# Kernel tuning notes

Hardware: AMD Instinct MI355X
Metric: run time of the kernel (lower is better)

## Reference

```python
import jax, jax.numpy as jnp
import numpy as np

NUM_EXPERTS = 64
INPUT_SIZE = 2048
NUM_TOKENS = 16384
TOPK = 8
INIT_STD = 0.02


def setup_inputs() -> dict:
    key = jax.random.key(0)
    k1, k2 = jax.random.split(key)
    input = jax.random.normal(k1, (NUM_TOKENS, INPUT_SIZE), dtype=jnp.float32)
    weight = INIT_STD * jax.random.normal(k2, (NUM_EXPERTS, INPUT_SIZE), dtype=jnp.float32)
    return {"input": input, "weight": weight}


def reference(input, weight):
    # gating GEMM: [N, D] x [E, D]^T -> [N, E]
    logits = jnp.einsum('nd,ed->ne', input, weight)
    n, e = logits.shape
    # pre_softmax=False branch: topk on raw logits, then softmax over selected
    top_scores, top_idx = jax.lax.top_k(logits, TOPK)          # [N, K]
    probs = jax.nn.softmax(top_scores.astype(jnp.float32), axis=-1).astype(logits.dtype)
    rows = jnp.arange(n)[:, None]                               # [N, 1]
    routing_probs = jnp.zeros_like(logits).at[rows, top_idx].set(probs)
    routing_map = jnp.zeros((n, e), dtype=jnp.bool_).at[rows, top_idx].set(True)
    return routing_probs, routing_map
```

## Files before the change

### kernel.cpp

```cpp
#include <hip/hip_runtime.h>
#include <cstdint>
#include <cmath>

#define D_DIM 2048
#define E_DIM 64
#define N_TOK 16384
#define K_TOP 8
#define KSTEP 32
#define TSTEPS 16
#define NFRAG 12

typedef __attribute__((ext_vector_type(8))) short bf16x8;
typedef __attribute__((ext_vector_type(4))) float f32x4;

__device__ inline void split3(const f32x4 v0, const f32x4 v1,
                              bf16x8& h, bf16x8& m, bf16x8& l) {
#pragma unroll
  for (int j = 0; j < 8; ++j) {
    const float x = (j < 4) ? v0[j] : v1[j - 4];
    const unsigned u = __builtin_bit_cast(unsigned, x);
    const unsigned rh = (u + 0x7FFFu + ((u >> 16) & 1u)) & 0xFFFF0000u;
    h[j] = (short)(rh >> 16);
    const float r1 = x - __builtin_bit_cast(float, rh);
    const unsigned u1 = __builtin_bit_cast(unsigned, r1);
    const unsigned rm = (u1 + 0x7FFFu + ((u1 >> 16) & 1u)) & 0xFFFF0000u;
    m[j] = (short)(rm >> 16);
    const float r2 = r1 - __builtin_bit_cast(float, rm);
    l[j] = (short)(__builtin_bit_cast(unsigned, r2) >> 16);
  }
}

__global__ void wprep_kernel(const float* __restrict__ W, uint4* __restrict__ WF) {
  const int gid = blockIdx.x * 256 + threadIdx.x;
  const int lane = gid & 63;
  const int et = (gid >> 6) & 3;
  const int ks = gid >> 8;
  const int e = et * 16 + (lane & 15);
  const int kg = lane >> 4;
  const float* src = W + (size_t)e * D_DIM + ks * KSTEP + kg * 8;
  const f32x4 a = *(const f32x4*)src;
  const f32x4 b = *(const f32x4*)(src + 4);
  bf16x8 h, m, l;
  split3(a, b, h, m, l);
  const int fbase = (ks * NFRAG + et * 3) * 64 + lane;
  WF[fbase] = __builtin_bit_cast(uint4, h);
  WF[fbase + 64] = __builtin_bit_cast(uint4, m);
  WF[fbase + 128] = __builtin_bit_cast(uint4, l);
}

#define BCV(x) __builtin_bit_cast(bf16x8, x)
#define MM(d, A, B) d = __builtin_amdgcn_mfma_f32_16x16x32_bf16(A, BCV(B), d, 0, 0, 0)

#define GL4(dst, voff, sbase, IMM)                              \
  asm volatile("global_load_dwordx4 %0, %1, %2 offset:" #IMM    \
               : "=v"(dst) : "v"(voff), "s"(sbase) : "memory")

#define SB0 __builtin_amdgcn_sched_barrier(0)
#define WAITV(N) asm volatile("s_waitcnt vmcnt(" #N ")" ::: "memory")
#define FENCE asm volatile("" ::: "memory")
#define BAR __builtin_amdgcn_s_barrier()

__global__ __launch_bounds__(256, 2)
void gemm_partial(const float* __restrict__ X, const uint4* __restrict__ WF,
                  float* __restrict__ Part) {
  __shared__ uint4 ldsB[4][NFRAG][64];

  const int bid = blockIdx.x;
  const int ks = bid & 3;
  const int mtile = bid >> 2;
  const int tid = threadIdx.x;
  const int w = tid >> 6;
  const int l = tid & 63;
  const int col = l & 15;
  const int kg = l >> 4;
  const int tokw = mtile * 128 + w * 32;

  const char* sX = (const char*)X + (size_t)(mtile * 128) * 8192 + (size_t)ks * 2048;
  const char* wfB = (const char*)WF + (size_t)ks * TSTEPS * 12288;

  const unsigned vX0 = (unsigned)(w * 32 * 8192 + col * 8192 + kg * 32);
  const unsigned vX1 = vX0 + 16 * 8192;

  f32x4 acc0[8], acc1[8];
#pragma unroll
  for (int i = 0; i < 8; ++i) { acc0[i] = (f32x4)0.f; acc1[i] = (f32x4)0.f; }

  f32x4 xE[4], xO[4];

#define LOADX(xS, t)                          \
  do {                                        \
    const char* sX_ = sX + (size_t)(t) * 128; \
    GL4(xS[0], vX0, sX_, 0);                  \
    GL4(xS[1], vX0, sX_, 16);                 \
    GL4(xS[2], vX1, sX_, 0);                  \
    GL4(xS[3], vX1, sX_, 16);                 \
  } while (0)

#define STAGE(t, buf)                                                        \
  do {                                                                       \
    _Pragma("unroll") for (int c = 0; c < 3; ++c) {                          \
      const int f_ = w * 3 + c;                                              \
      const char* g_ = wfB + (size_t)(t) * 12288 + f_ * 1024 + l * 16;       \
      __builtin_amdgcn_global_load_lds(                                      \
          (const __attribute__((address_space(1))) void*)g_,                 \
          (__attribute__((address_space(3))) void*)&ldsB[buf][f_][0], 16, 0, 0); \
    }                                                                        \
  } while (0)

#define CRUNCH(buf, xS)                                                      \
  do {                                                                       \
    bf16x8 ah0, am0, al0, ah1, am1, al1;                                     \
    split3(xS[0], xS[1], ah0, am0, al0);                                     \
    split3(xS[2], xS[3], ah1, am1, al1);                                     \
    const uint4* fb_ = &ldsB[buf][0][0];                                     \
    uint4 f0 = fb_[0 * 64 + l], f1 = fb_[1 * 64 + l], f2 = fb_[2 * 64 + l];  \
    uint4 f3 = fb_[3 * 64 + l], f4 = fb_[4 * 64 + l], f5 = fb_[5 * 64 + l];  \
    uint4 f6 = fb_[6 * 64 + l], f7 = fb_[7 * 64 + l], f8 = fb_[8 * 64 + l];  \
    uint4 f9 = fb_[9 * 64 + l], f10 = fb_[10 * 64 + l], f11 = fb_[11 * 64 + l]; \
    MM(acc0[0], ah0, f0); MM(acc0[4], ah1, f0);                              \
    MM(acc0[1], ah0, f3); MM(acc0[5], ah1, f3);                              \
    MM(acc0[2], ah0, f6); MM(acc0[6], ah1, f6);                              \
    MM(acc0[3], ah0, f9); MM(acc0[7], ah1, f9);                              \
    MM(acc1[0], ah0, f1); MM(acc1[4], ah1, f1);                              \
    MM(acc1[1], ah0, f4); MM(acc1[5], ah1, f4);                              \
    MM(acc1[2], ah0, f7); MM(acc1[6], ah1, f7);                              \
    MM(acc1[3], ah0, f10); MM(acc1[7], ah1, f10);                            \
    MM(acc1[0], am0, f0); MM(acc1[4], am1, f0);                              \
    MM(acc1[1], am0, f3); MM(acc1[5], am1, f3);                              \
    MM(acc1[2], am0, f6); MM(acc1[6], am1, f6);                              \
    MM(acc1[3], am0, f9); MM(acc1[7], am1, f9);                              \
    MM(acc1[0], ah0, f2); MM(acc1[4], ah1, f2);                              \
    MM(acc1[1], ah0, f5); MM(acc1[5], ah1, f5);                              \
    MM(acc1[2], ah0, f8); MM(acc1[6], ah1, f8);                              \
    MM(acc1[3], ah0, f11); MM(acc1[7], ah1, f11);                            \
    MM(acc1[0], al0, f0); MM(acc1[4], al1, f0);                              \
    MM(acc1[1], al0, f3); MM(acc1[5], al1, f3);                              \
    MM(acc1[2], al0, f6); MM(acc1[6], al1, f6);                              \
    MM(acc1[3], al0, f9); MM(acc1[7], al1, f9);                              \
    MM(acc1[0], am0, f1); MM(acc1[4], am1, f1);                              \
    MM(acc1[1], am0, f4); MM(acc1[5], am1, f4);                              \
    MM(acc1[2], am0, f7); MM(acc1[6], am1, f7);                              \
    MM(acc1[3], am0, f10); MM(acc1[7], am1, f10);                            \
  } while (0)

  STAGE(0, 0);
  STAGE(1, 1);
  LOADX(xE, 0);
  LOADX(xO, 1);

#pragma unroll 1
  for (int t = 0; t < TSTEPS - 2; t += 2) {
    STAGE(t + 2, (t + 2) & 3);
    WAITV(7);
    SB0;
    FENCE; BAR; FENCE;
    CRUNCH(t & 3, xE);
    LOADX(xE, t + 2);
    STAGE(t + 3, (t + 3) & 3);
    WAITV(7);
    SB0;
    FENCE; BAR; FENCE;
    CRUNCH((t + 1) & 3, xO);
    LOADX(xO, t + 3);
  }
  WAITV(4);
  SB0;
  FENCE; BAR; FENCE;
  CRUNCH(2, xE);
  WAITV(0);
  SB0;
  FENCE; BAR; FENCE;
  CRUNCH(3, xO);

#pragma unroll
  for (int half = 0; half < 2; ++half)
#pragma unroll
    for (int q = 0; q < 4; ++q) {
      const int tok = tokw + half * 16 + kg * 4 + q;
      float* dst = Part + ((size_t)ks * N_TOK + tok) * E_DIM + col;
#pragma unroll
      for (int et = 0; et < 4; ++et)
        dst[et * 16] = acc0[half * 4 + et][q] + acc1[half * 4 + et][q];
    }
}

__global__ __launch_bounds__(256)
void reduce_router(const float* __restrict__ Part,
                   float* __restrict__ Pout, float* __restrict__ Mout) {
  const int lane = threadIdx.x & 63;
  const int gw = blockIdx.x * 4 + (threadIdx.x >> 6);

#pragma unroll 1
  for (int j = 0; j < 8; ++j) {
    const int tok = gw * 8 + j;
    const size_t base = (size_t)tok * E_DIM + lane;
    float v = Part[base];
    v += Part[(size_t)1 * N_TOK * E_DIM + base];
    v += Part[(size_t)2 * N_TOK * E_DIM + base];
    v += Part[(size_t)3 * N_TOK * E_DIM + base];

    float topv[K_TOP];
    int topi[K_TOP];
#pragma unroll
    for (int kk = 0; kk < K_TOP; ++kk) {
      float m = v;
#pragma unroll
      for (int off = 32; off > 0; off >>= 1)
        m = fmaxf(m, __shfl_xor(m, off, 64));
      const unsigned long long bal = __ballot(v == m);
      const int li = __ffsll(bal) - 1;
      topv[kk] = m;
      topi[kk] = li;
      if (lane == li) v = -INFINITY;
    }

    float p[K_TOP], sum = 0.f;
#pragma unroll
    for (int kk = 0; kk < K_TOP; ++kk) {
      p[kk] = expf(topv[kk] - topv[0]);
      sum += p[kk];
    }
    const float inv = 1.f / sum;

    float pv = 0.f, mv = 0.f;
#pragma unroll
    for (int kk = 0; kk < K_TOP; ++kk)
      if (topi[kk] == lane) { pv = p[kk] * inv; mv = 1.f; }

    Pout[(size_t)tok * E_DIM + lane] = pv;
    Mout[(size_t)tok * E_DIM + lane] = mv;
  }
}

extern "C" void kernel_launch(void* const* d_in, const int* in_sizes, int n_in,
                              void* d_out, int out_size, void* d_ws, size_t ws_size,
                              hipStream_t stream) {
  const float* X = (const float*)d_in[0];
  const float* W = (const float*)d_in[1];
  float* P = (float*)d_out;
  float* M = P + (size_t)N_TOK * E_DIM;

  uint4* WF = (uint4*)d_ws;
  float* Part = (float*)((char*)d_ws + (size_t)(1 << 20));

  wprep_kernel<<<dim3(64), dim3(256), 0, stream>>>(W, WF);
  gemm_partial<<<dim3(512), dim3(256), 0, stream>>>(X, WF, Part);
  reduce_router<<<dim3(512), dim3(256), 0, stream>>>(Part, P, M);
}
```

Measured before the change: 59.20 us.

## Halve LDS buffering and regroup fragment loads to fit three blocks per CU

Cuts the weight-fragment LDS ring from four to two buffers and restructures the pipeline so each stage is issued after the barrier into the just-freed buffer. CRUNCH now loads only four fragments at a time, grouped by hi/mid/lo part, to shorten register live ranges, and launch bounds ask for three blocks per CU. The reduce kernel processes four tokens per wave with twice as many blocks. The gain is occupancy, at the cost of a shallower prefetch depth that may expose load latency.

```diff
diff --git a/kernel.cpp b/kernel.cpp
--- a/kernel.cpp
+++ b/kernel.cpp
@@ -60,10 +60,10 @@
 #define FENCE asm volatile("" ::: "memory")
 #define BAR __builtin_amdgcn_s_barrier()
 
-__global__ __launch_bounds__(256, 2)
+__global__ __launch_bounds__(256, 3)
 void gemm_partial(const float* __restrict__ X, const uint4* __restrict__ WF,
                   float* __restrict__ Part) {
-  __shared__ uint4 ldsB[4][NFRAG][64];
+  __shared__ uint4 ldsB[2][NFRAG][64];
 
   const int bid = blockIdx.x;
   const int ks = bid & 3;
@@ -107,70 +107,78 @@
     }                                                                        \
   } while (0)
 
-#define CRUNCH(buf, xS)                                                      \
-  do {                                                                       \
-    bf16x8 ah0, am0, al0, ah1, am1, al1;                                     \
-    split3(xS[0], xS[1], ah0, am0, al0);                                     \
-    split3(xS[2], xS[3], ah1, am1, al1);                                     \
-    const uint4* fb_ = &ldsB[buf][0][0];                                     \
-    uint4 f0 = fb_[0 * 64 + l], f1 = fb_[1 * 64 + l], f2 = fb_[2 * 64 + l];  \
-    uint4 f3 = fb_[3 * 64 + l], f4 = fb_[4 * 64 + l], f5 = fb_[5 * 64 + l];  \
-    uint4 f6 = fb_[6 * 64 + l], f7 = fb_[7 * 64 + l], f8 = fb_[8 * 64 + l];  \
-    uint4 f9 = fb_[9 * 64 + l], f10 = fb_[10 * 64 + l], f11 = fb_[11 * 64 + l]; \
-    MM(acc0[0], ah0, f0); MM(acc0[4], ah1, f0);                              \
-    MM(acc0[1], ah0, f3); MM(acc0[5], ah1, f3);                              \
-    MM(acc0[2], ah0, f6); MM(acc0[6], ah1, f6);                              \
-    MM(acc0[3], ah0, f9); MM(acc0[7], ah1, f9);                              \
-    MM(acc1[0], ah0, f1); MM(acc1[4], ah1, f1);                              \
-    MM(acc1[1], ah0, f4); MM(acc1[5], ah1, f4);                              \
-    MM(acc1[2], ah0, f7); MM(acc1[6], ah1, f7);                              \
-    MM(acc1[3], ah0, f10); MM(acc1[7], ah1, f10);                            \
-    MM(acc1[0], am0, f0); MM(acc1[4], am1, f0);                              \
-    MM(acc1[1], am0, f3); MM(acc1[5], am1, f3);                              \
-    MM(acc1[2], am0, f6); MM(acc1[6], am1, f6);                              \
-    MM(acc1[3], am0, f9); MM(acc1[7], am1, f9);                              \
-    MM(acc1[0], ah0, f2); MM(acc1[4], ah1, f2);                              \
-    MM(acc1[1], ah0, f5); MM(acc1[5], ah1, f5);                              \
-    MM(acc1[2], ah0, f8); MM(acc1[6], ah1, f8);                              \
-    MM(acc1[3], ah0, f11); MM(acc1[7], ah1, f11);                            \
-    MM(acc1[0], al0, f0); MM(acc1[4], al1, f0);                              \
-    MM(acc1[1], al0, f3); MM(acc1[5], al1, f3);                              \
-    MM(acc1[2], al0, f6); MM(acc1[6], al1, f6);                              \
-    MM(acc1[3], al0, f9); MM(acc1[7], al1, f9);                              \
-    MM(acc1[0], am0, f1); MM(acc1[4], am1, f1);                              \
-    MM(acc1[1], am0, f4); MM(acc1[5], am1, f4);                              \
-    MM(acc1[2], am0, f7); MM(acc1[6], am1, f7);                              \
-    MM(acc1[3], am0, f10); MM(acc1[7], am1, f10);                            \
+#define CRUNCH(buf, xS)                                                            \
+  do {                                                                             \
+    bf16x8 ah0, am0, al0, ah1, am1, al1;                                           \
+    split3(xS[0], xS[1], ah0, am0, al0);                                           \
+    split3(xS[2], xS[3], ah1, am1, al1);                                           \
+    const uint4* fb_ = &ldsB[buf][0][0];                                           \
+    {                                                                              \
+      uint4 hh0 = fb_[0 * 64 + l], hh1 = fb_[3 * 64 + l];                          \
+      uint4 hh2 = fb_[6 * 64 + l], hh3 = fb_[9 * 64 + l];                          \
+      MM(acc0[0], ah0, hh0); MM(acc0[4], ah1, hh0);                                \
+      MM(acc0[1], ah0, hh1); MM(acc0[5], ah1, hh1);                                \
+      MM(acc0[2], ah0, hh2); MM(acc0[6], ah1, hh2);                                \
+      MM(acc0[3], ah0, hh3); MM(acc0[7], ah1, hh3);                                \
+      MM(acc1[0], am0, hh0); MM(acc1[4], am1, hh0);                                \
+      MM(acc1[1], am0, hh1); MM(acc1[5], am1, hh1);                                \
+      MM(acc1[2], am0, hh2); MM(acc1[6], am1, hh2);                                \
+      MM(acc1[3], am0, hh3); MM(acc1[7], am1, hh3);                                \
+      MM(acc1[0], al0, hh0); MM(acc1[4], al1, hh0);                                \
+      MM(acc1[1], al0, hh1); MM(acc1[5], al1, hh1);                                \
+      MM(acc1[2], al0, hh2); MM(acc1[6], al1, hh2);                                \
+      MM(acc1[3], al0, hh3); MM(acc1[7], al1, hh3);                                \
+    }                                                                              \
+    {                                                                              \
+      uint4 mm0 = fb_[1 * 64 + l], mm1 = fb_[4 * 64 + l];                          \
+      uint4 mm2 = fb_[7 * 64 + l], mm3 = fb_[10 * 64 + l];                         \
+      MM(acc1[0], ah0, mm0); MM(acc1[4], ah1, mm0);                                \
+      MM(acc1[1], ah0, mm1); MM(acc1[5], ah1, mm1);                                \
+      MM(acc1[2], ah0, mm2); MM(acc1[6], ah1, mm2);                                \
+      MM(acc1[3], ah0, mm3); MM(acc1[7], ah1, mm3);                                \
+      MM(acc1[0], am0, mm0); MM(acc1[4], am1, mm0);                                \
+      MM(acc1[1], am0, mm1); MM(acc1[5], am1, mm1);                                \
+      MM(acc1[2], am0, mm2); MM(acc1[6], am1, mm2);                                \
+      MM(acc1[3], am0, mm3); MM(acc1[7], am1, mm3);                                \
+    }                                                                              \
+    {                                                                              \
+      uint4 ll0 = fb_[2 * 64 + l], ll1 = fb_[5 * 64 + l];                          \
+      uint4 ll2 = fb_[8 * 64 + l], ll3 = fb_[11 * 64 + l];                         \
+      MM(acc1[0], ah0, ll0); MM(acc1[4], ah1, ll0);                                \
+      MM(acc1[1], ah0, ll1); MM(acc1[5], ah1, ll1);                                \
+      MM(acc1[2], ah0, ll2); MM(acc1[6], ah1, ll2);                                \
+      MM(acc1[3], ah0, ll3); MM(acc1[7], ah1, ll3);                                \
+    }                                                                              \
   } while (0)
 
   STAGE(0, 0);
-  STAGE(1, 1);
   LOADX(xE, 0);
   LOADX(xO, 1);
 
 #pragma unroll 1
   for (int t = 0; t < TSTEPS - 2; t += 2) {
-    STAGE(t + 2, (t + 2) & 3);
-    WAITV(7);
+    WAITV(4);
     SB0;
     FENCE; BAR; FENCE;
-    CRUNCH(t & 3, xE);
+    STAGE(t + 1, (t + 1) & 1);
+    CRUNCH(t & 1, xE);
     LOADX(xE, t + 2);
-    STAGE(t + 3, (t + 3) & 3);
-    WAITV(7);
+    WAITV(4);
     SB0;
     FENCE; BAR; FENCE;
-    CRUNCH((t + 1) & 3, xO);
+    STAGE(t + 2, (t + 2) & 1);
+    CRUNCH((t + 1) & 1, xO);
     LOADX(xO, t + 3);
   }
   WAITV(4);
   SB0;
   FENCE; BAR; FENCE;
-  CRUNCH(2, xE);
+  STAGE(15, 1);
+  CRUNCH(0, xE);
   WAITV(0);
   SB0;
   FENCE; BAR; FENCE;
-  CRUNCH(3, xO);
+  CRUNCH(1, xO);
 
 #pragma unroll
   for (int half = 0; half < 2; ++half)
@@ -191,8 +199,8 @@
   const int gw = blockIdx.x * 4 + (threadIdx.x >> 6);
 
 #pragma unroll 1
-  for (int j = 0; j < 8; ++j) {
-    const int tok = gw * 8 + j;
+  for (int j = 0; j < 4; ++j) {
+    const int tok = gw * 4 + j;
     const size_t base = (size_t)tok * E_DIM + lane;
     float v = Part[base];
     v += Part[(size_t)1 * N_TOK * E_DIM + base];
@@ -245,5 +253,5 @@
 
   wprep_kernel<<<dim3(64), dim3(256), 0, stream>>>(W, WF);
   gemm_partial<<<dim3(512), dim3(256), 0, stream>>>(X, WF, Part);
-  reduce_router<<<dim3(512), dim3(256), 0, stream>>>(Part, P, M);
-}
+  reduce_router<<<dim3(1024), dim3(256), 0, stream>>>(Part, P, M);
+}
```

After: 73.35 us. 1.24x slower.
